# Performance work log

Measured on AMD Instinct MI355X. Metric: run time of the kernel, lower is better.

The kernel has to match this reference:

```python
import jax, jax.numpy as jnp
import numpy as np

N_NODES, N_EDGES = 20000, 100000
HEADS, OUT = 4, 256
HID = 256


def setup_inputs() -> dict:
    key = jax.random.key(0)
    ks = jax.random.split(key, 16)
    g = lambda k, shp, fan: jax.random.normal(k, shp, jnp.float32) * (1.0 / np.sqrt(fan))
    return {
        "x": jax.random.normal(ks[0], (N_NODES, 7), jnp.float32),
        "edge_attr": jax.random.normal(ks[1], (N_EDGES, 7), jnp.float32),
        "W_ne": g(ks[2], (7, HID), 7), "b_ne": jnp.zeros((HID,), jnp.float32),
        "W_ee": g(ks[3], (7, HID), 7), "b_ee": jnp.zeros((HID,), jnp.float32),
        "W_l": g(ks[4], (HID, HEADS * OUT), HID), "b_l": jnp.zeros((HEADS * OUT,), jnp.float32),
        "W_r": g(ks[5], (HID, HEADS * OUT), HID), "b_r": jnp.zeros((HEADS * OUT,), jnp.float32),
        "W_e": g(ks[6], (HID, HEADS * OUT), HID), "b_e": jnp.zeros((HEADS * OUT,), jnp.float32),
        "att": g(ks[7], (HEADS, OUT), OUT),
        "conv_bias": jnp.zeros((HEADS * OUT,), jnp.float32),
        "W_d1": g(ks[8], (HEADS * OUT, HID), HEADS * OUT), "b_d1": jnp.zeros((HID,), jnp.float32),
        "W_d2": g(ks[9], (HID, 6), HID), "b_d2": jnp.zeros((6,), jnp.float32),
        "edge_index": jax.random.randint(ks[10], (2, N_EDGES), 0, N_NODES, jnp.int64),
    }


def reference(x, edge_attr, W_ne, b_ne, W_ee, b_ee, W_l, b_l, W_r, b_r,
              W_e, b_e, att, conv_bias, W_d1, b_d1, W_d2, b_d2, edge_index):
    N = x.shape[0]
    src, dst = edge_index[0], edge_index[1]

    # node / edge encoders: Linear + ReLU
    h = jax.nn.relu(x @ W_ne + b_ne)                 # [N, 256]
    e = jax.nn.relu(edge_attr @ W_ee + b_ee)         # [E, 256]

    # GATv2 with edge features
    x_l = (h @ W_l + b_l).reshape(N, HEADS, OUT)     # source transform
    x_r = (h @ W_r + b_r).reshape(N, HEADS, OUT)     # target transform
    e_h = (e @ W_e + b_e).reshape(-1, HEADS, OUT)    # [E, H, C]

    z = jax.nn.leaky_relu(x_l[src] + x_r[dst] + e_h, 0.2)   # [E, H, C]
    logits = jnp.einsum('ehc,hc->eh', z, att)                # [E, H]

    # segment softmax over incoming edges of each target node (numerically stable)
    m = jax.ops.segment_max(logits, dst, num_segments=N)     # [N, H]
    m = jnp.where(jnp.isfinite(m), m, 0.0)
    expv = jnp.exp(logits - m[dst])                          # [E, H]
    denom = jax.ops.segment_sum(expv, dst, num_segments=N)   # [N, H]
    denom = jnp.where(denom == 0.0, 1.0, denom)
    alpha = expv / denom[dst]                                # [E, H]

    msg = x_l[src] * alpha[:, :, None]                       # [E, H, C]
    agg = jax.ops.segment_sum(msg, dst, num_segments=N)      # [N, H, C]
    node_enc = agg.reshape(N, HEADS * OUT) + conv_bias       # concat heads

    # decoder MLP; mode != 'train' -> sigmoid
    pred = jax.nn.relu(node_enc @ W_d1 + b_d1) @ W_d2 + b_d2
    return jax.nn.sigmoid(pred)                              # [N, 6]
```

## Files before the change

kernel.cpp:

```cpp
#include <hip/hip_runtime.h>
#include <hip/hip_bf16.h>

#define NN 20000
#define NE 100000
#define HID 256
#define HO 1024
#define HEADS 4
#define OUT 256

typedef __attribute__((ext_vector_type(8))) short bf16x8;
typedef __attribute__((ext_vector_type(4))) float f32x4;

__device__ inline ushort f2bf(float f) {
    union { float f; unsigned u; } v; v.f = f;
    unsigned r = v.u + 0x7FFFu + ((v.u >> 16) & 1u);
    return (ushort)(r >> 16);
}
__device__ inline float bf2f(ushort b) {
    union { unsigned u; float f; } v; v.u = ((unsigned)b) << 16;
    return v.f;
}

__global__ __launch_bounds__(256) void node_enc_kernel(
    const float* __restrict__ x, const float* __restrict__ W,
    const float* __restrict__ b, ushort* __restrict__ h)
{
    int n = blockIdx.x;
    int c = threadIdx.x;
    __shared__ float xs[8];
    if (threadIdx.x < 7) xs[threadIdx.x] = x[n * 7 + threadIdx.x];
    __syncthreads();
    float acc = b[c];
#pragma unroll
    for (int k = 0; k < 7; k++) acc += xs[k] * W[k * HID + c];
    h[(size_t)n * HID + c] = f2bf(fmaxf(acc, 0.f));
}

__global__ __launch_bounds__(256) void transpose_bf16_kernel(
    const float* __restrict__ W, ushort* __restrict__ WT, int K, int N)
{
    int k = blockIdx.x;
    int n = blockIdx.y * 256 + threadIdx.x;
    WT[(size_t)n * K + k] = f2bf(W[(size_t)k * N + n]);
}

__global__ __launch_bounds__(256) void biasH_kernel(
    const float* __restrict__ conv_bias, const float* __restrict__ W_d1,
    const float* __restrict__ b_d1, float* __restrict__ biasH)
{
    int c = threadIdx.x;
    float acc = b_d1[c];
    for (int k = 0; k < HO; k++) acc += conv_bias[k] * W_d1[(size_t)k * HID + c];
    biasH[c] = acc;
}

__global__ __launch_bounds__(256) void hist_kernel(
    const int* __restrict__ ei, int* __restrict__ deg)
{
    int e = blockIdx.x * blockDim.x + threadIdx.x;
    if (e >= NE) return;
    atomicAdd(&deg[ei[NE + e]], 1);
}

__global__ __launch_bounds__(1024) void scan_kernel(
    const int* __restrict__ deg, int* __restrict__ rowptr, int* __restrict__ cursor)
{
    const int CH = 20;
    int t = threadIdx.x;
    int start = t * CH;
    int d[CH];
    int local = 0;
#pragma unroll
    for (int i = 0; i < CH; i++) {
        int idx = start + i;
        d[i] = (idx < NN) ? deg[idx] : 0;
        local += d[i];
    }
    int incl = local;
#pragma unroll
    for (int off = 1; off < 64; off <<= 1) {
        int v = __shfl_up(incl, off);
        if ((t & 63) >= off) incl += v;
    }
    __shared__ int waveTot[16];
    int wv = t >> 6;
    if ((t & 63) == 63) waveTot[wv] = incl;
    __syncthreads();
    if (t < 16) {
        int v = waveTot[t];
        int s = v;
#pragma unroll
        for (int off = 1; off < 16; off <<= 1) {
            int u = __shfl_up(s, off);
            if (t >= off) s += u;
        }
        waveTot[t] = s - v;
    }
    __syncthreads();
    int run = (incl - local) + waveTot[wv];
#pragma unroll
    for (int i = 0; i < CH; i++) {
        int idx = start + i;
        if (idx < NN) { rowptr[idx] = run; cursor[idx] = run; }
        run += d[i];
    }
    if (t == 1023) rowptr[NN] = run;
}

__global__ __launch_bounds__(256) void scatter_kernel(
    const int* __restrict__ ei, int* __restrict__ cursor, int* __restrict__ eidx,
    int* __restrict__ srcs, int* __restrict__ dsts)
{
    int e = blockIdx.x * blockDim.x + threadIdx.x;
    if (e >= NE) return;
    int d = ei[NE + e];
    int pos = atomicAdd(&cursor[d], 1);
    eidx[pos] = e;
    srcs[pos] = ei[e];
    dsts[pos] = d;
}

__global__ __launch_bounds__(256) void qkv_gemm_kernel(
    const ushort* __restrict__ A, const ushort* __restrict__ BT,
    const float* __restrict__ bias, ushort* __restrict__ C, int M)
{
    __shared__ __align__(16) ushort As[64][264];
    int t = threadIdx.x, w = t >> 6, lane = t & 63;
    int l15 = lane & 15, l4 = lane >> 4;
    int row0 = blockIdx.x * 64;
    int colOff = blockIdx.y * 256;
    {
        int r = t >> 2, c0 = (t & 3) * 64;
        int row = row0 + r;
        if (row < M) {
            const ushort* src = &A[(size_t)row * 256 + c0];
#pragma unroll
            for (int c = 0; c < 8; c++)
                *(bf16x8*)&As[r][c0 + c * 8] = *(const bf16x8*)&src[c * 8];
        } else {
            bf16x8 z = (bf16x8){0, 0, 0, 0, 0, 0, 0, 0};
#pragma unroll
            for (int c = 0; c < 8; c++) *(bf16x8*)&As[r][c0 + c * 8] = z;
        }
    }
    __syncthreads();
    f32x4 acc[4][4] = {};
    for (int k0 = 0; k0 < 256; k0 += 32) {
        bf16x8 a[4], b[4];
#pragma unroll
        for (int rt = 0; rt < 4; rt++)
            a[rt] = *(const bf16x8*)&As[rt * 16 + l15][k0 + l4 * 8];
#pragma unroll
        for (int ct = 0; ct < 4; ct++) {
            int n = colOff + w * 64 + ct * 16 + l15;
            b[ct] = *(const bf16x8*)&BT[(size_t)n * 256 + k0 + l4 * 8];
        }
#pragma unroll
        for (int rt = 0; rt < 4; rt++)
#pragma unroll
            for (int ct = 0; ct < 4; ct++)
                acc[rt][ct] = __builtin_amdgcn_mfma_f32_16x16x32_bf16(
                    a[rt], b[ct], acc[rt][ct], 0, 0, 0);
    }
    float bv[4];
#pragma unroll
    for (int ct = 0; ct < 4; ct++) bv[ct] = bias[colOff + w * 64 + ct * 16 + l15];
#pragma unroll
    for (int rt = 0; rt < 4; rt++)
#pragma unroll
        for (int ct = 0; ct < 4; ct++)
#pragma unroll
            for (int r = 0; r < 4; r++) {
                int row = row0 + rt * 16 + l4 * 4 + r;
                if (row < M)
                    C[(size_t)row * 1024 + colOff + w * 64 + ct * 16 + l15] =
                        f2bf(acc[rt][ct][r] + bv[ct]);
            }
}

__global__ __launch_bounds__(256) void dec_gemm_kernel(
    const ushort* __restrict__ A, const ushort* __restrict__ BT,
    const float* __restrict__ biasH, ushort* __restrict__ C, int M)
{
    __shared__ __align__(16) ushort As[64][264];
    int t = threadIdx.x, w = t >> 6, lane = t & 63;
    int l15 = lane & 15, l4 = lane >> 4;
    int row0 = blockIdx.x * 64;
    f32x4 acc[4][4] = {};
    for (int kc = 0; kc < 4; kc++) {
        if (kc) __syncthreads();
        {
            int r = t >> 2, c0 = (t & 3) * 64;
            int row = row0 + r;
            if (row < M) {
                const ushort* src = &A[(size_t)row * 1024 + kc * 256 + c0];
#pragma unroll
                for (int c = 0; c < 8; c++)
                    *(bf16x8*)&As[r][c0 + c * 8] = *(const bf16x8*)&src[c * 8];
            } else {
                bf16x8 z = (bf16x8){0, 0, 0, 0, 0, 0, 0, 0};
#pragma unroll
                for (int c = 0; c < 8; c++) *(bf16x8*)&As[r][c0 + c * 8] = z;
            }
        }
        __syncthreads();
        for (int k0 = 0; k0 < 256; k0 += 32) {
            bf16x8 a[4], b[4];
#pragma unroll
            for (int rt = 0; rt < 4; rt++)
                a[rt] = *(const bf16x8*)&As[rt * 16 + l15][k0 + l4 * 8];
#pragma unroll
            for (int ct = 0; ct < 4; ct++) {
                int n = w * 64 + ct * 16 + l15;
                b[ct] = *(const bf16x8*)&BT[(size_t)n * 1024 + kc * 256 + k0 + l4 * 8];
            }
#pragma unroll
            for (int rt = 0; rt < 4; rt++)
#pragma unroll
                for (int ct = 0; ct < 4; ct++)
                    acc[rt][ct] = __builtin_amdgcn_mfma_f32_16x16x32_bf16(
                        a[rt], b[ct], acc[rt][ct], 0, 0, 0);
        }
    }
    float bv[4];
#pragma unroll
    for (int ct = 0; ct < 4; ct++) bv[ct] = biasH[w * 64 + ct * 16 + l15];
#pragma unroll
    for (int rt = 0; rt < 4; rt++)
#pragma unroll
        for (int ct = 0; ct < 4; ct++)
#pragma unroll
            for (int r = 0; r < 4; r++) {
                int row = row0 + rt * 16 + l4 * 4 + r;
                if (row < M)
                    C[(size_t)row * 256 + w * 64 + ct * 16 + l15] =
                        f2bf(fmaxf(acc[rt][ct][r] + bv[ct], 0.f));
            }
}

#define EPB 32
__global__ __launch_bounds__(256, 4) void edge_mfma_logits_kernel(
    const float* __restrict__ edge_attr, const float* __restrict__ W_ee,
    const float* __restrict__ b_ee, const ushort* __restrict__ WeT,
    const float* __restrict__ b_e, const float* __restrict__ att,
    const ushort* __restrict__ xl, const ushort* __restrict__ xr,
    const int* __restrict__ eidx, const int* __restrict__ srcs,
    const int* __restrict__ dsts, float* __restrict__ lbuf4)
{
    __shared__ __align__(16) ushort As[EPB][264];
    __shared__ __align__(16) ushort XLR[64][264];
    __shared__ float ea[EPB * 7];
    __shared__ int sArr[EPB], dArr[EPB];
    __shared__ float red[4][EPB];
    int j0 = blockIdx.x * EPB;
    int t = threadIdx.x, w = t >> 6, lane = t & 63;
    int l15 = lane & 15, l4 = lane >> 4;

    if (t < EPB * 7) {
        int e = eidx[j0 + t / 7];
        ea[t] = edge_attr[(size_t)e * 7 + t % 7];
    }
    if (t < EPB) {
        sArr[t] = srcs[j0 + t];
        dArr[t] = dsts[j0 + t];
    }
    __syncthreads();

    {
        float w7[7];
#pragma unroll
        for (int k = 0; k < 7; k++) w7[k] = W_ee[k * HID + t];
        float bee = b_ee[t];
#pragma unroll 4
        for (int r = 0; r < EPB; r++) {
            float acc = bee;
#pragma unroll
            for (int k = 0; k < 7; k++) acc += w7[k] * ea[r * 7 + k];
            As[r][t] = f2bf(fmaxf(acc, 0.f));
        }
    }
    __syncthreads();

    int gr = t >> 2;
    int gc = (t & 3) * 64;
    int eIdx = gr & 31;

    for (int h = 0; h < HEADS; h++) {
        f32x4 acc[2][4] = {};
        for (int k0 = 0; k0 < 256; k0 += 32) {
            bf16x8 a[2], b[4];
#pragma unroll
            for (int rt = 0; rt < 2; rt++)
                a[rt] = *(const bf16x8*)&As[rt * 16 + l15][k0 + l4 * 8];
#pragma unroll
            for (int ct = 0; ct < 4; ct++) {
                int n = h * 256 + w * 64 + ct * 16 + l15;
                b[ct] = *(const bf16x8*)&WeT[(size_t)n * 256 + k0 + l4 * 8];
            }
#pragma unroll
            for (int rt = 0; rt < 2; rt++)
#pragma unroll
                for (int ct = 0; ct < 4; ct++)
                    acc[rt][ct] = __builtin_amdgcn_mfma_f32_16x16x32_bf16(
                        a[rt], b[ct], acc[rt][ct], 0, 0, 0);
        }

        {
            const ushort* src = (gr < 32)
                ? &xl[(size_t)sArr[eIdx] * 1024 + h * 256 + gc]
                : &xr[(size_t)dArr[eIdx] * 1024 + h * 256 + gc];
#pragma unroll
            for (int c = 0; c < 8; c++)
                *(bf16x8*)&XLR[gr][gc + c * 8] = *(const bf16x8*)&src[c * 8];
        }

        float bev[4], atv[4];
#pragma unroll
        for (int ct = 0; ct < 4; ct++) {
            int col = w * 64 + ct * 16 + l15;
            bev[ct] = b_e[h * 256 + col];
            atv[ct] = att[h * 256 + col];
        }
        __syncthreads();

        float lp[2][4];
#pragma unroll
        for (int rt = 0; rt < 2; rt++)
#pragma unroll
            for (int r = 0; r < 4; r++) {
                int li = rt * 16 + l4 * 4 + r;
                float p = 0.f;
#pragma unroll
                for (int ct = 0; ct < 4; ct++) {
                    int col = w * 64 + ct * 16 + l15;
                    float z = acc[rt][ct][r] + bev[ct] +
                              bf2f(XLR[li][col]) + bf2f(XLR[32 + li][col]);
                    z = (z > 0.f) ? z : 0.2f * z;
                    p += z * atv[ct];
                }
                lp[rt][r] = p;
            }
#pragma unroll
        for (int off = 1; off < 16; off <<= 1)
#pragma unroll
            for (int rt = 0; rt < 2; rt++)
#pragma unroll
                for (int r = 0; r < 4; r++)
                    lp[rt][r] += __shfl_xor(lp[rt][r], off);
        if (l15 == 0)
#pragma unroll
            for (int rt = 0; rt < 2; rt++)
#pragma unroll
                for (int r = 0; r < 4; r++)
                    red[w][rt * 16 + l4 * 4 + r] = lp[rt][r];
        __syncthreads();

        if (t < EPB) {
            float v = red[0][t] + red[1][t] + red[2][t] + red[3][t];
            lbuf4[(size_t)(j0 + t) * 4 + h] = v;
        }
    }
}

__global__ __launch_bounds__(256) void softmax_agg_kernel(
    const float* __restrict__ lbuf4, const int* __restrict__ rowptr,
    const int* __restrict__ srcs, const ushort* __restrict__ xl,
    ushort* __restrict__ agg)
{
    int n = blockIdx.x;
    int h = threadIdx.x >> 6, lane = threadIdx.x & 63;
    int r0 = rowptr[n], r1 = rowptr[n + 1];
    float m = -3.4e38f;
    for (int j = r0; j < r1; j++)
        m = fmaxf(m, lbuf4[(size_t)j * 4 + h]);
    float denom = 0.f;
    for (int j = r0; j < r1; j++)
        denom += __expf(lbuf4[(size_t)j * 4 + h] - m);
    float rd = (denom > 0.f) ? 1.f / denom : 0.f;
    float a0 = 0.f, a1 = 0.f, a2 = 0.f, a3 = 0.f;
    for (int j = r0; j < r1; j++) {
        int s = srcs[j];
        float alpha = __expf(lbuf4[(size_t)j * 4 + h] - m) * rd;
        ushort4 xv = *(const ushort4*)&xl[(size_t)s * 1024 + h * 256 + lane * 4];
        a0 += alpha * bf2f(xv.x); a1 += alpha * bf2f(xv.y);
        a2 += alpha * bf2f(xv.z); a3 += alpha * bf2f(xv.w);
    }
    ushort4 o;
    o.x = f2bf(a0); o.y = f2bf(a1); o.z = f2bf(a2); o.w = f2bf(a3);
    *(ushort4*)&agg[(size_t)n * 1024 + h * 256 + lane * 4] = o;
}

__global__ __launch_bounds__(256) void final_kernel(
    const ushort* __restrict__ hid, const float* __restrict__ W_d2,
    const float* __restrict__ b_d2, float* __restrict__ out)
{
    int g = blockIdx.x * blockDim.x + threadIdx.x;
    if (g >= NN * 6) return;
    int n = g / 6, j = g % 6;
    float acc = b_d2[j];
    const bf16x8* hp = reinterpret_cast<const bf16x8*>(&hid[(size_t)n * HID]);
#pragma unroll 4
    for (int k8 = 0; k8 < HID / 8; k8++) {
        bf16x8 hv = hp[k8];
#pragma unroll
        for (int i = 0; i < 8; i++)
            acc += bf2f((ushort)hv[i]) * W_d2[(k8 * 8 + i) * 6 + j];
    }
    out[g] = 1.f / (1.f + __expf(-acc));
}

extern "C" void kernel_launch(void* const* d_in, const int* in_sizes, int n_in,
                              void* d_out, int out_size, void* d_ws, size_t ws_size,
                              hipStream_t stream)
{
    const float* x         = (const float*)d_in[0];
    const float* edge_attr = (const float*)d_in[1];
    const float* W_ne = (const float*)d_in[2];  const float* b_ne = (const float*)d_in[3];
    const float* W_ee = (const float*)d_in[4];  const float* b_ee = (const float*)d_in[5];
    const float* W_l  = (const float*)d_in[6];  const float* b_l  = (const float*)d_in[7];
    const float* W_r  = (const float*)d_in[8];  const float* b_r  = (const float*)d_in[9];
    const float* W_e  = (const float*)d_in[10]; const float* b_e  = (const float*)d_in[11];
    const float* att  = (const float*)d_in[12];
    const float* conv_bias = (const float*)d_in[13];
    const float* W_d1 = (const float*)d_in[14]; const float* b_d1 = (const float*)d_in[15];
    const float* W_d2 = (const float*)d_in[16]; const float* b_d2 = (const float*)d_in[17];
    const int*   ei   = (const int*)d_in[18];
    float* out = (float*)d_out;

    const size_t NODE256  = (size_t)NN * HID;
    const size_t NODE1024 = (size_t)NN * HO;
    char* p = (char*)d_ws;
    ushort* h_bf   = (ushort*)p;  p += NODE256 * 2;
    ushort* xl_bf  = (ushort*)p;  p += NODE1024 * 2;
    ushort* xr_bf  = (ushort*)p;  p += NODE1024 * 2;
    float*  lbuf4  = (float*)p;   p += (size_t)NE * HEADS * 4;
    int*    deg    = (int*)p;     p += (size_t)NN * 4;
    int*    rowptr = (int*)p;     p += (size_t)(NN + 1) * 4;
    int*    cursor = (int*)p;     p += (size_t)NN * 4;
    int*    eidx   = (int*)p;     p += (size_t)NE * 4;
    int*    srcs   = (int*)p;     p += (size_t)NE * 4;
    int*    dsts   = (int*)p;     p += (size_t)NE * 4;
    float*  biasH  = (float*)p;   p += HID * 4;
    ushort* WlT    = (ushort*)p;  p += (size_t)HO * HID * 2;
    ushort* WrT    = (ushort*)p;  p += (size_t)HO * HID * 2;
    ushort* WeT    = (ushort*)p;  p += (size_t)HO * HID * 2;
    ushort* Wd1T   = (ushort*)p;  p += (size_t)HID * HO * 2;
    if ((size_t)(p - (char*)d_ws) > ws_size) return;

    ushort* agg_bf = xr_bf;
    ushort* hid_bf = h_bf;

    hipMemsetAsync(deg, 0, (size_t)NN * 4, stream);

    node_enc_kernel<<<NN, 256, 0, stream>>>(x, W_ne, b_ne, h_bf);
    biasH_kernel<<<1, 256, 0, stream>>>(conv_bias, W_d1, b_d1, biasH);

    transpose_bf16_kernel<<<dim3(HID, HO / 256), 256, 0, stream>>>(W_l,  WlT,  HID, HO);
    transpose_bf16_kernel<<<dim3(HID, HO / 256), 256, 0, stream>>>(W_r,  WrT,  HID, HO);
    transpose_bf16_kernel<<<dim3(HID, HO / 256), 256, 0, stream>>>(W_e,  WeT,  HID, HO);
    transpose_bf16_kernel<<<dim3(HO, HID / 256), 256, 0, stream>>>(W_d1, Wd1T, HO,  HID);

    hist_kernel<<<(NE + 255) / 256, 256, 0, stream>>>(ei, deg);
    scan_kernel<<<1, 1024, 0, stream>>>(deg, rowptr, cursor);
    scatter_kernel<<<(NE + 255) / 256, 256, 0, stream>>>(ei, cursor, eidx, srcs, dsts);

    const int gemmGrid = (NN + 63) / 64;

    qkv_gemm_kernel<<<dim3(gemmGrid, 4), 256, 0, stream>>>(h_bf, WlT, b_l, xl_bf, NN);
    qkv_gemm_kernel<<<dim3(gemmGrid, 4), 256, 0, stream>>>(h_bf, WrT, b_r, xr_bf, NN);

    edge_mfma_logits_kernel<<<NE / EPB, 256, 0, stream>>>(
        edge_attr, W_ee, b_ee, WeT, b_e, att, xl_bf, xr_bf,
        eidx, srcs, dsts, lbuf4);

    softmax_agg_kernel<<<NN, 256, 0, stream>>>(lbuf4, rowptr, srcs, xl_bf, agg_bf);

    dec_gemm_kernel<<<gemmGrid, 256, 0, stream>>>(agg_bf, Wd1T, biasH, hid_bf, NN);

    final_kernel<<<(NN * 6 + 255) / 256, 256, 0, stream>>>(hid_bf, W_d2, b_d2, out);
}
```

Before: 568.3 us.

## Give each wave full head width and 16 edges in edge logits kernel

The edge logits kernel now processes 64 edges per block. Each wave owns 16 edges across all 256 columns of a head, so the per-edge dot-product reduction finishes inside the wave with shuffles. This removes the XLR shared-memory staging of gathered x_l/x_r rows, the cross-wave reduction buffer, and two block barriers per head, and halves the grid. The trade-off is 16 accumulator tiles per wave, a heavy unrolled loop that raises register pressure, and x_l/x_r/bias/att values read directly from global memory with 2-byte scalar loads instead of vectorised staging.

```diff
diff --git a/kernel.cpp b/kernel.cpp
--- a/kernel.cpp
+++ b/kernel.cpp
@@ -238,7 +238,7 @@
             }
 }
 
-#define EPB 32
+#define EPB64 64
 __global__ __launch_bounds__(256, 4) void edge_mfma_logits_kernel(
     const float* __restrict__ edge_attr, const float* __restrict__ W_ee,
     const float* __restrict__ b_ee, const ushort* __restrict__ WeT,
@@ -247,22 +247,23 @@
     const int* __restrict__ eidx, const int* __restrict__ srcs,
     const int* __restrict__ dsts, float* __restrict__ lbuf4)
 {
-    __shared__ __align__(16) ushort As[EPB][264];
-    __shared__ __align__(16) ushort XLR[64][264];
-    __shared__ float ea[EPB * 7];
-    __shared__ int sArr[EPB], dArr[EPB];
-    __shared__ float red[4][EPB];
-    int j0 = blockIdx.x * EPB;
+    __shared__ __align__(16) ushort As[EPB64][264];
+    __shared__ float ea[EPB64 * 7];
+    __shared__ int sArr[EPB64], dArr[EPB64];
+    int j0 = blockIdx.x * EPB64;
+    int nval = NE - j0; if (nval > EPB64) nval = EPB64;
     int t = threadIdx.x, w = t >> 6, lane = t & 63;
     int l15 = lane & 15, l4 = lane >> 4;
 
-    if (t < EPB * 7) {
-        int e = eidx[j0 + t / 7];
-        ea[t] = edge_attr[(size_t)e * 7 + t % 7];
-    }
-    if (t < EPB) {
-        sArr[t] = srcs[j0 + t];
-        dArr[t] = dsts[j0 + t];
+    for (int i = t; i < EPB64 * 7; i += 256) {
+        int ji = i / 7;
+        int jc = (ji < nval) ? ji : 0;
+        ea[i] = (ji < nval) ? edge_attr[(size_t)eidx[j0 + jc] * 7 + i % 7] : 0.f;
+    }
+    if (t < EPB64) {
+        int jc = (t < nval) ? t : 0;
+        sArr[t] = srcs[j0 + jc];
+        dArr[t] = dsts[j0 + jc];
     }
     __syncthreads();
 
@@ -272,7 +273,7 @@
         for (int k = 0; k < 7; k++) w7[k] = W_ee[k * HID + t];
         float bee = b_ee[t];
 #pragma unroll 4
-        for (int r = 0; r < EPB; r++) {
+        for (int r = 0; r < EPB64; r++) {
             float acc = bee;
 #pragma unroll
             for (int k = 0; k < 7; k++) acc += w7[k] * ea[r * 7 + k];
@@ -281,83 +282,40 @@
     }
     __syncthreads();
 
-    int gr = t >> 2;
-    int gc = (t & 3) * 64;
-    int eIdx = gr & 31;
-
     for (int h = 0; h < HEADS; h++) {
-        f32x4 acc[2][4] = {};
+        f32x4 acc[16];
+#pragma unroll
+        for (int ct = 0; ct < 16; ct++) acc[ct] = (f32x4){0.f, 0.f, 0.f, 0.f};
+#pragma unroll
         for (int k0 = 0; k0 < 256; k0 += 32) {
-            bf16x8 a[2], b[4];
-#pragma unroll
-            for (int rt = 0; rt < 2; rt++)
-                a[rt] = *(const bf16x8*)&As[rt * 16 + l15][k0 + l4 * 8];
-#pragma unroll
-            for (int ct = 0; ct < 4; ct++) {
-                int n = h * 256 + w * 64 + ct * 16 + l15;
-                b[ct] = *(const bf16x8*)&WeT[(size_t)n * 256 + k0 + l4 * 8];
-            }
-#pragma unroll
-            for (int rt = 0; rt < 2; rt++)
-#pragma unroll
-                for (int ct = 0; ct < 4; ct++)
-                    acc[rt][ct] = __builtin_amdgcn_mfma_f32_16x16x32_bf16(
-                        a[rt], b[ct], acc[rt][ct], 0, 0, 0);
-        }
-
-        {
-            const ushort* src = (gr < 32)
-                ? &xl[(size_t)sArr[eIdx] * 1024 + h * 256 + gc]
-                : &xr[(size_t)dArr[eIdx] * 1024 + h * 256 + gc];
-#pragma unroll
-            for (int c = 0; c < 8; c++)
-                *(bf16x8*)&XLR[gr][gc + c * 8] = *(const bf16x8*)&src[c * 8];
-        }
-
-        float bev[4], atv[4];
-#pragma unroll
-        for (int ct = 0; ct < 4; ct++) {
-            int col = w * 64 + ct * 16 + l15;
-            bev[ct] = b_e[h * 256 + col];
-            atv[ct] = att[h * 256 + col];
-        }
-        __syncthreads();
-
-        float lp[2][4];
-#pragma unroll
-        for (int rt = 0; rt < 2; rt++)
-#pragma unroll
-            for (int r = 0; r < 4; r++) {
-                int li = rt * 16 + l4 * 4 + r;
-                float p = 0.f;
-#pragma unroll
-                for (int ct = 0; ct < 4; ct++) {
-                    int col = w * 64 + ct * 16 + l15;
-                    float z = acc[rt][ct][r] + bev[ct] +
-                              bf2f(XLR[li][col]) + bf2f(XLR[32 + li][col]);
-                    z = (z > 0.f) ? z : 0.2f * z;
-                    p += z * atv[ct];
-                }
-                lp[rt][r] = p;
-            }
-#pragma unroll
-        for (int off = 1; off < 16; off <<= 1)
-#pragma unroll
-            for (int rt = 0; rt < 2; rt++)
-#pragma unroll
-                for (int r = 0; r < 4; r++)
-                    lp[rt][r] += __shfl_xor(lp[rt][r], off);
-        if (l15 == 0)
-#pragma unroll
-            for (int rt = 0; rt < 2; rt++)
-#pragma unroll
-                for (int r = 0; r < 4; r++)
-                    red[w][rt * 16 + l4 * 4 + r] = lp[rt][r];
-        __syncthreads();
-
-        if (t < EPB) {
-            float v = red[0][t] + red[1][t] + red[2][t] + red[3][t];
-            lbuf4[(size_t)(j0 + t) * 4 + h] = v;
+            bf16x8 a = *(const bf16x8*)&As[w * 16 + l15][k0 + l4 * 8];
+#pragma unroll
+            for (int ct = 0; ct < 16; ct++) {
+                bf16x8 b = *(const bf16x8*)
+                    &WeT[(size_t)(h * 256 + ct * 16 + l15) * 256 + k0 + l4 * 8];
+                acc[ct] = __builtin_amdgcn_mfma_f32_16x16x32_bf16(a, b, acc[ct], 0, 0, 0);
+            }
+        }
+
+        const float* beh = &b_e[h * 256];
+        const float* ath = &att[h * 256];
+#pragma unroll
+        for (int r = 0; r < 4; r++) {
+            int le = w * 16 + l4 * 4 + r;
+            const ushort* xlp = &xl[(size_t)sArr[le] * 1024 + h * 256];
+            const ushort* xrp = &xr[(size_t)dArr[le] * 1024 + h * 256];
+            float p = 0.f;
+#pragma unroll
+            for (int ct = 0; ct < 16; ct++) {
+                int col = ct * 16 + l15;
+                float z = acc[ct][r] + beh[col] + bf2f(xlp[col]) + bf2f(xrp[col]);
+                z = (z > 0.f) ? z : 0.2f * z;
+                p += z * ath[col];
+            }
+#pragma unroll
+            for (int off = 1; off < 16; off <<= 1) p += __shfl_xor(p, off);
+            if (l15 == 0 && le < nval)
+                lbuf4[(size_t)(j0 + le) * 4 + h] = p;
         }
     }
 }
@@ -469,7 +427,7 @@
     qkv_gemm_kernel<<<dim3(gemmGrid, 4), 256, 0, stream>>>(h_bf, WlT, b_l, xl_bf, NN);
     qkv_gemm_kernel<<<dim3(gemmGrid, 4), 256, 0, stream>>>(h_bf, WrT, b_r, xr_bf, NN);
 
-    edge_mfma_logits_kernel<<<NE / EPB, 256, 0, stream>>>(
+    edge_mfma_logits_kernel<<<(NE + EPB64 - 1) / EPB64, 256, 0, stream>>>(
         edge_attr, W_ee, b_ee, WeT, b_e, att, xl_bf, xr_bf,
         eidx, srcs, dsts, lbuf4);
 
```

Measured after the change: 889.7 us. 56.6% more time.
